# Kernel tuning notes

Hardware: AMD Instinct MI355X
Metric: run time of the kernel (lower is better)

## Reference

```python
import jax, jax.numpy as jnp
import numpy as np

B, S, D_IN = 4, 2048, 1024
N_HEAD, D_ATTN, D_OUT = 16, 64, 1024
D_H = N_HEAD * D_ATTN  # 1024; NOTE: no head split in original module


def setup_inputs() -> dict:
    key = jax.random.key(0)
    ks = jax.random.split(key, 12)
    s = 1.0 / np.sqrt(D_IN)
    inp = {
        "q": jax.random.normal(ks[0], (B, S, D_IN), dtype=jnp.float32),
        "k": jax.random.normal(ks[1], (B, S, D_IN), dtype=jnp.float32),
        "v": jax.random.normal(ks[2], (B, S, D_IN), dtype=jnp.float32),
        "mask": jax.random.randint(ks[3], (B, S, S), 0, 2, dtype=jnp.int32),
        "Wq": jax.random.normal(ks[4], (D_H, D_IN), dtype=jnp.float32) * s,
        "bq": jnp.zeros((D_H,), dtype=jnp.float32),
        "Wk": jax.random.normal(ks[5], (D_H, D_IN), dtype=jnp.float32) * s,
        "bk": jnp.zeros((D_H,), dtype=jnp.float32),
        "Wv": jax.random.normal(ks[6], (D_H, D_IN), dtype=jnp.float32) * s,
        "bv": jnp.zeros((D_H,), dtype=jnp.float32),
        "Wo": jax.random.normal(ks[7], (D_OUT, D_H), dtype=jnp.float32) * (1.0 / np.sqrt(D_H)),
        "bo": jnp.zeros((D_OUT,), dtype=jnp.float32),
    }
    return inp


def reference(q, k, v, mask, Wq, bq, Wk, bk, Wv, bv, Wo, bo):
    # manual QKV projections (torch Linear: x @ W.T + b)
    Q = q @ Wq.T + bq  # [B,S,D_H]
    K = k @ Wk.T + bk
    V = v @ Wv.T + bv
    d_k = Q.shape[-1]  # full concatenated dim (no head split, faithful)
    e = jnp.einsum("bsd,btd->bst", Q, K) / jnp.sqrt(jnp.float32(d_k))  # [B,S,S]
    MASK_FILL = jnp.float32(-(2 ** 15))  # original uses -2**15 regardless of dtype
    e = jnp.where(mask == 0, MASK_FILL, e)
    a = jax.nn.softmax(e, axis=-1)
    y = jnp.einsum("bst,btd->bsd", a, V)  # [B,S,D_H]
    return y @ Wo.T + bo  # [B,S,D_OUT]
```

## Files before the change

kernel.cpp:

```cpp
#include <hip/hip_runtime.h>
#include <hip/hip_bf16.h>

#define B_   4
#define S_   2048
#define DIN  1024
#define DH   1024
#define DOUT 1024

typedef __attribute__((ext_vector_type(8))) __bf16 bf16x8;
typedef __attribute__((ext_vector_type(4))) float floatx4;
typedef __attribute__((ext_vector_type(4))) float f32x4;
typedef __attribute__((ext_vector_type(4))) u_short u16x4;
typedef unsigned short u16;
typedef unsigned int u32;
typedef unsigned long long u64;

__device__ inline u16 f2bf(float f) {
  union { float f; u32 u; } x; x.f = f;
  u32 r = x.u + 0x7fffu + ((x.u >> 16) & 1u);
  return (u16)(r >> 16);
}

#define GLOAD(SRC, DST) __builtin_amdgcn_global_load_lds(                     \
    (const __attribute__((address_space(1))) u32*)(SRC),                      \
    (__attribute__((address_space(3))) u32*)(DST), 16, 0, 0)
#define WAITVM0() asm volatile("s_waitcnt vmcnt(0)" ::: "memory")

__global__ __launch_bounds__(256)
void cast_all(const float* __restrict__ q, const float* __restrict__ k,
              const float* __restrict__ v, const float* __restrict__ w0,
              const float* __restrict__ w1, const float* __restrict__ w2,
              const float* __restrict__ w3, u16* __restrict__ dst) {
  const long nQ = (long)B_ * S_ * DIN;
  const long nW = (long)DH * DIN;
  long b = blockIdx.x;
  const float* src; long doff;
  if (b < 8192)       { src = q;  doff = 0;            }
  else if (b < 16384) { src = k;  doff = nQ;     b -= 8192;  }
  else if (b < 24576) { src = v;  doff = 2 * nQ; b -= 16384; }
  else if (b < 25600) { src = w0; doff = 3 * nQ; b -= 24576; }
  else if (b < 26624) { src = w1; doff = 3 * nQ + nW;     b -= 25600; }
  else if (b < 27648) { src = w2; doff = 3 * nQ + 2 * nW; b -= 26624; }
  else                { src = w3; doff = 3 * nQ + 3 * nW; b -= 27648; }
  long i = b * 256 + threadIdx.x;
  f32x4 vv = __builtin_nontemporal_load(((const f32x4*)src) + i);
  u16x4 o;
  o.x = f2bf(vv.x); o.y = f2bf(vv.y); o.z = f2bf(vv.z); o.w = f2bf(vv.w);
  ((u16x4*)(dst + doff))[i] = o;
}

__global__ __launch_bounds__(256)
void mask_pack(const int* __restrict__ mask, u64* __restrict__ packed) {
  const long i = (long)blockIdx.x * 256 + threadIdx.x;
  const int mk = __builtin_nontemporal_load(mask + i);
  const u64 bal = __ballot(mk != 0);
  if ((threadIdx.x & 63) == 0) packed[i >> 6] = bal;
}

__global__ __launch_bounds__(256)
void transpose_bf16(const u16* __restrict__ in, u16* __restrict__ out) {
  __shared__ u16 t[32][33];
  const int b = blockIdx.z;
  const int r0 = blockIdx.y * 32, c0 = blockIdx.x * 32;
  const int tx = threadIdx.x & 31, ty = threadIdx.x >> 5;
  const u16* ib = in + (long)b * S_ * DH;
  u16* ob = out + (long)b * DH * S_;
#pragma unroll
  for (int i = 0; i < 4; ++i) {
    int r = ty + i * 8;
    t[r][tx] = ib[(long)(r0 + r) * DH + (c0 + tx)];
  }
  __syncthreads();
#pragma unroll
  for (int i = 0; i < 4; ++i) {
    int r = ty + i * 8;
    ob[(long)(c0 + r) * S_ + (r0 + tx)] = t[tx][r];
  }
}

#define EPI_BF16_BIAS     0
#define EPI_BF16_ROWSCALE 1
#define EPI_F32_BIAS      2

template <int EPI>
__global__ __launch_bounds__(256, 4)
void gemm97(const u16* __restrict__ A, const u16* __restrict__ Bm,
            void* __restrict__ C,
            const float* __restrict__ bias0, const float* __restrict__ bias1,
            const float* __restrict__ bias2,
            const float* __restrict__ Psum,
            int M, int N, int K,
            long sA, long sB, long sC,
            int nbx, int nby) {
  __shared__ u16 lds_[16384];
  __shared__ float invs_s[(EPI == EPI_BF16_ROWSCALE) ? 128 : 1];

  const int tid = threadIdx.x;
  const int w = tid >> 6, l = tid & 63;
  const int wr = w >> 1, wc = w & 1;
  const int lr = l & 15, q = l >> 4;

  const int flat = blockIdx.x;
  const int swz = (flat & 7) * ((int)gridDim.x >> 3) + (flat >> 3);
  const int bx = swz % nbx;
  const int rest = swz / nbx;
  const int by = rest % nby;
  const int bz = rest / nby;

  const long arow0 = (long)by * 128;
  const long bcol0 = (long)bx * 128;
  const u16* Ab = A + bz * sA + arow0 * K;
  const u16* Bb = Bm + bz * sB + bcol0 * K;
  const int nt = K >> 6;

  if constexpr (EPI == EPI_BF16_ROWSCALE) {
    if (tid < 128) {
      const float4* p = (const float4*)(Psum + ((long)bz * S_ + arow0 + tid) * 16);
      float4 a = p[0], b = p[1], c = p[2], d = p[3];
      float s = (a.x + a.y + a.z + a.w) + (b.x + b.y + b.z + b.w)
              + (c.x + c.y + c.z + c.w) + (d.x + d.y + d.z + d.w);
      invs_s[tid] = 1.0f / s;
    }
  }

  const int st_r = tid >> 3;
  const int st_ks = (tid & 7) ^ (st_r & 7);

  floatx4 acc[4][4] = {};

  for (int t = 0; t < nt; ++t) {
    const long k0 = (long)t << 6;
#pragma unroll
    for (int i = 0; i < 4; ++i)
      GLOAD(Ab + (long)(i * 32 + st_r) * K + k0 + st_ks * 8,
            &lds_[i * 2048 + tid * 8]);
#pragma unroll
    for (int i = 0; i < 4; ++i)
      GLOAD(Bb + (long)(i * 32 + st_r) * K + k0 + st_ks * 8,
            &lds_[8192 + i * 2048 + tid * 8]);
    WAITVM0();
    __syncthreads();

    bf16x8 a[4][2], b[4][2];
#pragma unroll
    for (int m = 0; m < 4; ++m)
#pragma unroll
      for (int kk = 0; kk < 2; ++kk) {
        const int r = wr * 64 + m * 16 + lr, s = kk * 4 + q;
        a[m][kk] = *(const bf16x8*)&lds_[r * 64 + ((s ^ (r & 7)) * 8)];
      }
#pragma unroll
    for (int n = 0; n < 4; ++n)
#pragma unroll
      for (int kk = 0; kk < 2; ++kk) {
        const int c = wc * 64 + n * 16 + lr, s = kk * 4 + q;
        b[n][kk] = *(const bf16x8*)&lds_[8192 + c * 64 + ((s ^ (c & 7)) * 8)];
      }
#pragma unroll
    for (int kk = 0; kk < 2; ++kk)
#pragma unroll
      for (int n = 0; n < 4; ++n)
#pragma unroll
        for (int m = 0; m < 4; ++m)
          acc[m][n] = __builtin_amdgcn_mfma_f32_16x16x32_bf16(
              a[m][kk], b[n][kk], acc[m][n], 0, 0, 0);
    __syncthreads();
  }

  const int r4 = q * 4;
  const float* bp = bias0;
  if constexpr (EPI == EPI_BF16_BIAS)
    bp = (bz == 0) ? bias0 : ((bz == 1) ? bias1 : bias2);
#pragma unroll
  for (int mf = 0; mf < 4; ++mf)
#pragma unroll
    for (int nf = 0; nf < 4; ++nf)
#pragma unroll
      for (int r = 0; r < 4; ++r) {
        const long row = arow0 + wr * 64 + mf * 16 + r4 + r;
        const long col = bcol0 + wc * 64 + nf * 16 + lr;
        float v = acc[mf][nf][r];
        if constexpr (EPI == EPI_BF16_BIAS) {
          v += bp[col];
          ((u16*)C)[bz * sC + row * N + col] = f2bf(v);
        } else if constexpr (EPI == EPI_BF16_ROWSCALE) {
          v *= invs_s[wr * 64 + mf * 16 + r4 + r];
          ((u16*)C)[bz * sC + row * N + col] = f2bf(v);
        } else {
          v += bp[col];
          ((float*)C)[bz * sC + row * N + col] = v;
        }
      }
}

__global__ __launch_bounds__(256, 4)
void pexp128(const u16* __restrict__ Q, const u16* __restrict__ Kb_,
             u16* __restrict__ P, const u32* __restrict__ packed,
             float* __restrict__ Psum) {
  __shared__ u16 lds_[16384];

  const int tid = threadIdx.x;
  const int w = tid >> 6, l = tid & 63;
  const int wr = w >> 1, wc = w & 1;
  const int lr = l & 15, q = l >> 4;

  const int flat = blockIdx.x;
  const int swz = (flat & 7) * ((int)gridDim.x >> 3) + (flat >> 3);
  const int bx = swz & 15;
  const int rest = swz >> 4;
  const int by = rest & 15;
  const int bz = rest >> 4;

  const long arow0 = (long)by * 128;
  const long bcol0 = (long)bx * 128;
  const int K = DH;
  const u16* Ab = Q + (long)bz * S_ * DH + arow0 * K;
  const u16* Bb = Kb_ + (long)bz * S_ * DH + bcol0 * K;

  const int st_r = tid >> 3;
  const int st_ks = (tid & 7) ^ (st_r & 7);

  floatx4 acc[4][4] = {};

#pragma unroll 4
  for (int t = 0; t < 16; ++t) {
    const long k0 = (long)t << 6;
#pragma unroll
    for (int i = 0; i < 4; ++i)
      GLOAD(Ab + (long)(i * 32 + st_r) * K + k0 + st_ks * 8,
            &lds_[i * 2048 + tid * 8]);
#pragma unroll
    for (int i = 0; i < 4; ++i)
      GLOAD(Bb + (long)(i * 32 + st_r) * K + k0 + st_ks * 8,
            &lds_[8192 + i * 2048 + tid * 8]);
    WAITVM0();
    __syncthreads();

    bf16x8 a[4][2], b[4][2];
#pragma unroll
    for (int m = 0; m < 4; ++m)
#pragma unroll
      for (int kk = 0; kk < 2; ++kk) {
        const int r = wr * 64 + m * 16 + lr, s = kk * 4 + q;
        a[m][kk] = *(const bf16x8*)&lds_[r * 64 + ((s ^ (r & 7)) * 8)];
      }
#pragma unroll
    for (int n = 0; n < 4; ++n)
#pragma unroll
      for (int kk = 0; kk < 2; ++kk) {
        const int c = wc * 64 + n * 16 + lr, s = kk * 4 + q;
        b[n][kk] = *(const bf16x8*)&lds_[8192 + c * 64 + ((s ^ (c & 7)) * 8)];
      }
#pragma unroll
    for (int kk = 0; kk < 2; ++kk)
#pragma unroll
      for (int n = 0; n < 4; ++n)
#pragma unroll
        for (int m = 0; m < 4; ++m)
          acc[m][n] = __builtin_amdgcn_mfma_f32_16x16x32_bf16(
              a[m][kk], b[n][kk], acc[m][n], 0, 0, 0);
    __syncthreads();
  }

  u32* pw = (u32*)&lds_[8192];
  {
    const u32* pg = packed + (long)bz * S_ * (S_ / 32)
                  + arow0 * (S_ / 32) + (bcol0 >> 5);
    const int lrow = tid >> 1;
    const int j0 = (tid & 1) * 2;
    pw[lrow * 4 + j0]     = pg[(long)lrow * (S_ / 32) + j0];
    pw[lrow * 4 + j0 + 1] = pg[(long)lrow * (S_ / 32) + j0 + 1];
  }
  __syncthreads();

  const int r4 = q * 4;
  float rsum[4][4];
#pragma unroll
  for (int mf = 0; mf < 4; ++mf)
#pragma unroll
    for (int r = 0; r < 4; ++r) rsum[mf][r] = 0.f;

#pragma unroll
  for (int mf = 0; mf < 4; ++mf)
#pragma unroll
    for (int r = 0; r < 4; ++r) {
      const int lrow = wr * 64 + mf * 16 + r4 + r;
      const long row = arow0 + lrow;
#pragma unroll
      for (int nf = 0; nf < 4; ++nf) {
        const u32 word = pw[lrow * 4 + wc * 2 + (nf >> 1)];
        const int bitpos = (nf & 1) * 16 + lr;
        const long col = bcol0 + wc * 64 + nf * 16 + lr;
        float p = 0.f;
        if ((word >> bitpos) & 1u) p = __expf(acc[mf][nf][r] * 0.03125f);
        P[(long)bz * S_ * S_ + row * S_ + col] = f2bf(p);
        rsum[mf][r] += p;
      }
    }
  __syncthreads();

  float* sc = (float*)lds_;
#pragma unroll
  for (int mf = 0; mf < 4; ++mf)
#pragma unroll
    for (int r = 0; r < 4; ++r) {
      float s = rsum[mf][r];
      s += __shfl_xor(s, 1); s += __shfl_xor(s, 2);
      s += __shfl_xor(s, 4); s += __shfl_xor(s, 8);
      if (lr == 0) sc[(wr * 64 + mf * 16 + r4 + r) * 2 + wc] = s;
    }
  __syncthreads();
  if (tid < 128) {
    float tot = sc[tid * 2] + sc[tid * 2 + 1];
    Psum[((long)bz * S_ + arow0 + tid) * 16 + bx] = tot;
  }
}

extern "C" void kernel_launch(void* const* d_in, const int* in_sizes, int n_in,
                              void* d_out, int out_size, void* d_ws, size_t ws_size,
                              hipStream_t stream) {
  const float* q    = (const float*)d_in[0];
  const float* k    = (const float*)d_in[1];
  const float* v    = (const float*)d_in[2];
  const int*   mask = (const int*)d_in[3];
  const float* Wq   = (const float*)d_in[4];
  const float* bq   = (const float*)d_in[5];
  const float* Wk   = (const float*)d_in[6];
  const float* bk   = (const float*)d_in[7];
  const float* Wv   = (const float*)d_in[8];
  const float* bv   = (const float*)d_in[9];
  const float* Wo   = (const float*)d_in[10];
  const float* bo   = (const float*)d_in[11];

  const long BS = (long)B_ * S_;
  const long nQ = BS * DH;
  const long nW = (long)DH * DIN;
  const long nE = (long)B_ * S_ * S_;

  char* ws = (char*)d_ws;
  size_t off = 0;
  auto alloc = [&](size_t bytes) {
    void* p = ws + off; off += (bytes + 255) & ~(size_t)255; return p;
  };

  u16* qb   = (u16*)alloc(nQ * 2);
  u16* kb   = (u16*)alloc(nQ * 2);
  u16* vb   = (u16*)alloc(nQ * 2);
  u16* wqb  = (u16*)alloc(nW * 2);
  u16* wkb  = (u16*)alloc(nW * 2);
  u16* wvb  = (u16*)alloc(nW * 2);
  u16* wob  = (u16*)alloc(nW * 2);
  u16* Qb   = (u16*)alloc(nQ * 2);
  u16* Kbf  = (u16*)alloc(nQ * 2);
  u16* Vb   = (u16*)alloc(nQ * 2);
  u16* VT   = (u16*)alloc(nQ * 2);
  u16* P    = (u16*)alloc(nE * 2);
  u64* pk   = (u64*)alloc(nE / 8);
  float* Psum = (float*)alloc(BS * 16 * 4);
  u16* Yb  = vb;
  (void)kb; (void)wkb; (void)wvb;

  cast_all<<<dim3(28672), 256, 0, stream>>>(q, k, v, Wq, Wk, Wv, Wo, qb);
  mask_pack<<<dim3(65536), 256, 0, stream>>>(mask, pk);

  gemm97<EPI_BF16_BIAS><<<dim3(1536), 256, 0, stream>>>(qb, wqb, Qb,
      bq, bk, bv, nullptr, (int)BS, DH, DIN, nQ, nW, nQ, 8, 64);

  {
    dim3 g(DH / 32, S_ / 32, B_);
    transpose_bf16<<<g, 256, 0, stream>>>(Vb, VT);
  }

  pexp128<<<dim3(1024), 256, 0, stream>>>(Qb, Kbf, P, (const u32*)pk, Psum);

  gemm97<EPI_BF16_ROWSCALE><<<dim3(512), 256, 0, stream>>>(P, VT, Yb,
      nullptr, nullptr, nullptr, Psum, S_, DH, S_,
      (long)S_ * S_, (long)DH * S_, (long)S_ * DH, 8, 16);

  gemm97<EPI_F32_BIAS><<<dim3(512), 256, 0, stream>>>(Yb, wob, d_out,
      bo, nullptr, nullptr, nullptr, (int)BS, DOUT, DH, 0, 0, 0, 8, 64);
}
```

Measured before the change: 235.4 us.

## Fuse fp32-to-bf16 activation cast into QKV projection GEMM and vectorize mask packing

```diff
diff --git a/kernel.cpp b/kernel.cpp
--- a/kernel.cpp
+++ b/kernel.cpp
@@ -10,6 +10,7 @@
 typedef __attribute__((ext_vector_type(8))) __bf16 bf16x8;
 typedef __attribute__((ext_vector_type(4))) float floatx4;
 typedef __attribute__((ext_vector_type(4))) float f32x4;
+typedef __attribute__((ext_vector_type(4))) int i32x4;
 typedef __attribute__((ext_vector_type(4))) u_short u16x4;
 typedef unsigned short u16;
 typedef unsigned int u32;
@@ -27,34 +28,35 @@
 #define WAITVM0() asm volatile("s_waitcnt vmcnt(0)" ::: "memory")
 
 __global__ __launch_bounds__(256)
-void cast_all(const float* __restrict__ q, const float* __restrict__ k,
-              const float* __restrict__ v, const float* __restrict__ w0,
-              const float* __restrict__ w1, const float* __restrict__ w2,
-              const float* __restrict__ w3, u16* __restrict__ dst) {
-  const long nQ = (long)B_ * S_ * DIN;
+void wcast(const float* __restrict__ w0, const float* __restrict__ w1,
+           const float* __restrict__ w2, const float* __restrict__ w3,
+           u16* __restrict__ dst) {
   const long nW = (long)DH * DIN;
   long b = blockIdx.x;
-  const float* src; long doff;
-  if (b < 8192)       { src = q;  doff = 0;            }
-  else if (b < 16384) { src = k;  doff = nQ;     b -= 8192;  }
-  else if (b < 24576) { src = v;  doff = 2 * nQ; b -= 16384; }
-  else if (b < 25600) { src = w0; doff = 3 * nQ; b -= 24576; }
-  else if (b < 26624) { src = w1; doff = 3 * nQ + nW;     b -= 25600; }
-  else if (b < 27648) { src = w2; doff = 3 * nQ + 2 * nW; b -= 26624; }
-  else                { src = w3; doff = 3 * nQ + 3 * nW; b -= 27648; }
-  long i = b * 256 + threadIdx.x;
+  const int r = (int)(b >> 10);
+  const float* src = (r == 0) ? w0 : (r == 1) ? w1 : (r == 2) ? w2 : w3;
+  long i = (b & 1023) * 256 + threadIdx.x;
   f32x4 vv = __builtin_nontemporal_load(((const f32x4*)src) + i);
   u16x4 o;
   o.x = f2bf(vv.x); o.y = f2bf(vv.y); o.z = f2bf(vv.z); o.w = f2bf(vv.w);
-  ((u16x4*)(dst + doff))[i] = o;
+  ((u16x4*)(dst + (long)r * nW))[i] = o;
 }
 
 __global__ __launch_bounds__(256)
 void mask_pack(const int* __restrict__ mask, u64* __restrict__ packed) {
-  const long i = (long)blockIdx.x * 256 + threadIdx.x;
-  const int mk = __builtin_nontemporal_load(mask + i);
-  const u64 bal = __ballot(mk != 0);
-  if ((threadIdx.x & 63) == 0) packed[i >> 6] = bal;
+  const long f = (long)blockIdx.x * 256 + threadIdx.x;
+  i32x4 m4 = __builtin_nontemporal_load(((const i32x4*)mask) + f);
+  u64 b0 = __ballot(m4.x != 0);
+  u64 b1 = __ballot(m4.y != 0);
+  u64 b2 = __ballot(m4.z != 0);
+  u64 b3 = __ballot(m4.w != 0);
+  if ((threadIdx.x & 63) == 0) {
+    const long g = f >> 6;
+    ulonglong2 p01; p01.x = b0; p01.y = b1;
+    ulonglong2 p23; p23.x = b2; p23.y = b3;
+    ((ulonglong2*)(packed + g * 4))[0] = p01;
+    ((ulonglong2*)(packed + g * 4))[1] = p23;
+  }
 }
 
 __global__ __launch_bounds__(256)
@@ -82,10 +84,12 @@
 #define EPI_BF16_ROWSCALE 1
 #define EPI_F32_BIAS      2
 
-template <int EPI>
+template <int EPI, bool AF32>
 __global__ __launch_bounds__(256, 4)
-void gemm97(const u16* __restrict__ A, const u16* __restrict__ Bm,
-            void* __restrict__ C,
+void gemm97(const u16* __restrict__ A,
+            const float* __restrict__ Af0, const float* __restrict__ Af1,
+            const float* __restrict__ Af2,
+            const u16* __restrict__ Bm, void* __restrict__ C,
             const float* __restrict__ bias0, const float* __restrict__ bias1,
             const float* __restrict__ bias2,
             const float* __restrict__ Psum,
@@ -109,7 +113,14 @@
 
   const long arow0 = (long)by * 128;
   const long bcol0 = (long)bx * 128;
-  const u16* Ab = A + bz * sA + arow0 * K;
+  const u16* Ab = nullptr;
+  const float* Afp = nullptr;
+  if constexpr (AF32) {
+    const float* As = (bz == 0) ? Af0 : ((bz == 1) ? Af1 : Af2);
+    Afp = As + arow0 * K;
+  } else {
+    Ab = A + bz * sA + arow0 * K;
+  }
   const u16* Bb = Bm + bz * sB + bcol0 * K;
   const int nt = K >> 6;
 
@@ -130,15 +141,40 @@
 
   for (int t = 0; t < nt; ++t) {
     const long k0 = (long)t << 6;
-#pragma unroll
-    for (int i = 0; i < 4; ++i)
-      GLOAD(Ab + (long)(i * 32 + st_r) * K + k0 + st_ks * 8,
-            &lds_[i * 2048 + tid * 8]);
-#pragma unroll
-    for (int i = 0; i < 4; ++i)
-      GLOAD(Bb + (long)(i * 32 + st_r) * K + k0 + st_ks * 8,
-            &lds_[8192 + i * 2048 + tid * 8]);
-    WAITVM0();
+    if constexpr (AF32) {
+      f32x4 va[4][2];
+#pragma unroll
+      for (int i = 0; i < 4; ++i) {
+        const float* sp = Afp + (long)(i * 32 + st_r) * K + k0 + st_ks * 8;
+        va[i][0] = *(const f32x4*)sp;
+        va[i][1] = *(const f32x4*)(sp + 4);
+      }
+#pragma unroll
+      for (int i = 0; i < 4; ++i)
+        GLOAD(Bb + (long)(i * 32 + st_r) * K + k0 + st_ks * 8,
+              &lds_[8192 + i * 2048 + tid * 8]);
+#pragma unroll
+      for (int i = 0; i < 4; ++i) {
+        bf16x8 o;
+#pragma unroll
+        for (int j = 0; j < 4; ++j) {
+          o[j]     = (__bf16)va[i][0][j];
+          o[j + 4] = (__bf16)va[i][1][j];
+        }
+        *(bf16x8*)&lds_[i * 2048 + tid * 8] = o;
+      }
+      WAITVM0();
+    } else {
+#pragma unroll
+      for (int i = 0; i < 4; ++i)
+        GLOAD(Ab + (long)(i * 32 + st_r) * K + k0 + st_ks * 8,
+              &lds_[i * 2048 + tid * 8]);
+#pragma unroll
+      for (int i = 0; i < 4; ++i)
+        GLOAD(Bb + (long)(i * 32 + st_r) * K + k0 + st_ks * 8,
+              &lds_[8192 + i * 2048 + tid * 8]);
+      WAITVM0();
+    }
     __syncthreads();
 
     bf16x8 a[4][2], b[4][2];
@@ -264,12 +300,12 @@
 
   u32* pw = (u32*)&lds_[8192];
   {
-    const u32* pg = packed + (long)bz * S_ * (S_ / 32)
-                  + arow0 * (S_ / 32) + (bcol0 >> 5);
+    const int half = bx & 1;
     const int lrow = tid >> 1;
     const int j0 = (tid & 1) * 2;
-    pw[lrow * 4 + j0]     = pg[(long)lrow * (S_ / 32) + j0];
-    pw[lrow * 4 + j0 + 1] = pg[(long)lrow * (S_ / 32) + j0 + 1];
+    const long g = (long)bz * 16384 + (arow0 + lrow) * 8 + (bx >> 1);
+    pw[lrow * 4 + j0]     = packed[g * 8 + j0 * 2 + half];
+    pw[lrow * 4 + j0 + 1] = packed[g * 8 + (j0 + 1) * 2 + half];
   }
   __syncthreads();
 
@@ -286,10 +322,10 @@
     for (int r = 0; r < 4; ++r) {
       const int lrow = wr * 64 + mf * 16 + r4 + r;
       const long row = arow0 + lrow;
+      const u32 word = pw[lrow * 4 + (lr & 3)];
 #pragma unroll
       for (int nf = 0; nf < 4; ++nf) {
-        const u32 word = pw[lrow * 4 + wc * 2 + (nf >> 1)];
-        const int bitpos = (nf & 1) * 16 + lr;
+        const int bitpos = wc * 16 + nf * 4 + (lr >> 2);
         const long col = bcol0 + wc * 64 + nf * 16 + lr;
         float p = 0.f;
         if ((word >> bitpos) & 1u) p = __expf(acc[mf][nf][r] * 0.03125f);
@@ -343,13 +379,7 @@
     void* p = ws + off; off += (bytes + 255) & ~(size_t)255; return p;
   };
 
-  u16* qb   = (u16*)alloc(nQ * 2);
-  u16* kb   = (u16*)alloc(nQ * 2);
-  u16* vb   = (u16*)alloc(nQ * 2);
-  u16* wqb  = (u16*)alloc(nW * 2);
-  u16* wkb  = (u16*)alloc(nW * 2);
-  u16* wvb  = (u16*)alloc(nW * 2);
-  u16* wob  = (u16*)alloc(nW * 2);
+  u16* wqb  = (u16*)alloc(4 * nW * 2);
   u16* Qb   = (u16*)alloc(nQ * 2);
   u16* Kbf  = (u16*)alloc(nQ * 2);
   u16* Vb   = (u16*)alloc(nQ * 2);
@@ -357,14 +387,16 @@
   u16* P    = (u16*)alloc(nE * 2);
   u64* pk   = (u64*)alloc(nE / 8);
   float* Psum = (float*)alloc(BS * 16 * 4);
-  u16* Yb  = vb;
-  (void)kb; (void)wkb; (void)wvb;
-
-  cast_all<<<dim3(28672), 256, 0, stream>>>(q, k, v, Wq, Wk, Wv, Wo, qb);
-  mask_pack<<<dim3(65536), 256, 0, stream>>>(mask, pk);
-
-  gemm97<EPI_BF16_BIAS><<<dim3(1536), 256, 0, stream>>>(qb, wqb, Qb,
-      bq, bk, bv, nullptr, (int)BS, DH, DIN, nQ, nW, nQ, 8, 64);
+  u16* Yb   = (u16*)alloc(nQ * 2);
+  u16* wob  = wqb + 3 * nW;
+  (void)Kbf;
+
+  wcast<<<dim3(4096), 256, 0, stream>>>(Wq, Wk, Wv, Wo, wqb);
+  mask_pack<<<dim3(16384), 256, 0, stream>>>(mask, pk);
+
+  gemm97<EPI_BF16_BIAS, true><<<dim3(1536), 256, 0, stream>>>(
+      nullptr, q, k, v, wqb, Qb, bq, bk, bv, nullptr,
+      (int)BS, DH, DIN, 0, nW, nQ, 8, 64);
 
   {
     dim3 g(DH / 32, S_ / 32, B_);
@@ -373,10 +405,11 @@
 
   pexp128<<<dim3(1024), 256, 0, stream>>>(Qb, Kbf, P, (const u32*)pk, Psum);
 
-  gemm97<EPI_BF16_ROWSCALE><<<dim3(512), 256, 0, stream>>>(P, VT, Yb,
-      nullptr, nullptr, nullptr, Psum, S_, DH, S_,
-      (long)S_ * S_, (long)DH * S_, (long)S_ * DH, 8, 16);
-
-  gemm97<EPI_F32_BIAS><<<dim3(512), 256, 0, stream>>>(Yb, wob, d_out,
-      bo, nullptr, nullptr, nullptr, (int)BS, DOUT, DH, 0, 0, 0, 8, 64);
-}
+  gemm97<EPI_BF16_ROWSCALE, false><<<dim3(512), 256, 0, stream>>>(
+      P, nullptr, nullptr, nullptr, VT, Yb, nullptr, nullptr, nullptr, Psum,
+      S_, DH, S_, (long)S_ * S_, (long)DH * S_, (long)S_ * DH, 8, 16);
+
+  gemm97<EPI_F32_BIAS, false><<<dim3(512), 256, 0, stream>>>(
+      Yb, nullptr, nullptr, nullptr, wob, d_out, bo, nullptr, nullptr, nullptr,
+      (int)BS, DOUT, DH, 0, 0, 0, 8, 64);
+}
```

After: 241.2 us. 1.02x slower.

## Fuse fp32-to-bf16 activation cast into QKV projection GEMM A-tile loads

Applied to the files above, without the earlier changes.

```diff
diff --git a/kernel.cpp b/kernel.cpp
--- a/kernel.cpp
+++ b/kernel.cpp
@@ -27,26 +27,18 @@
 #define WAITVM0() asm volatile("s_waitcnt vmcnt(0)" ::: "memory")
 
 __global__ __launch_bounds__(256)
-void cast_all(const float* __restrict__ q, const float* __restrict__ k,
-              const float* __restrict__ v, const float* __restrict__ w0,
-              const float* __restrict__ w1, const float* __restrict__ w2,
-              const float* __restrict__ w3, u16* __restrict__ dst) {
-  const long nQ = (long)B_ * S_ * DIN;
+void wcast(const float* __restrict__ w0, const float* __restrict__ w1,
+           const float* __restrict__ w2, const float* __restrict__ w3,
+           u16* __restrict__ dst) {
   const long nW = (long)DH * DIN;
   long b = blockIdx.x;
-  const float* src; long doff;
-  if (b < 8192)       { src = q;  doff = 0;            }
-  else if (b < 16384) { src = k;  doff = nQ;     b -= 8192;  }
-  else if (b < 24576) { src = v;  doff = 2 * nQ; b -= 16384; }
-  else if (b < 25600) { src = w0; doff = 3 * nQ; b -= 24576; }
-  else if (b < 26624) { src = w1; doff = 3 * nQ + nW;     b -= 25600; }
-  else if (b < 27648) { src = w2; doff = 3 * nQ + 2 * nW; b -= 26624; }
-  else                { src = w3; doff = 3 * nQ + 3 * nW; b -= 27648; }
-  long i = b * 256 + threadIdx.x;
+  const int r = (int)(b >> 10);
+  const float* src = (r == 0) ? w0 : (r == 1) ? w1 : (r == 2) ? w2 : w3;
+  long i = (b & 1023) * 256 + threadIdx.x;
   f32x4 vv = __builtin_nontemporal_load(((const f32x4*)src) + i);
   u16x4 o;
   o.x = f2bf(vv.x); o.y = f2bf(vv.y); o.z = f2bf(vv.z); o.w = f2bf(vv.w);
-  ((u16x4*)(dst + doff))[i] = o;
+  ((u16x4*)(dst + (long)r * nW))[i] = o;
 }
 
 __global__ __launch_bounds__(256)
@@ -78,7 +70,110 @@
   }
 }
 
-#define EPI_BF16_BIAS     0
+__global__ __launch_bounds__(256, 3)
+void gemm97f(const float* __restrict__ Af0, const float* __restrict__ Af1,
+             const float* __restrict__ Af2,
+             const u16* __restrict__ Bm, u16* __restrict__ C,
+             const float* __restrict__ bias0, const float* __restrict__ bias1,
+             const float* __restrict__ bias2,
+             int M, int N, int K, long sB, long sC,
+             int nbx, int nby) {
+  __shared__ u16 lds_[24576];
+
+  const int tid = threadIdx.x;
+  const int w = tid >> 6, l = tid & 63;
+  const int wr = w >> 1, wc = w & 1;
+  const int lr = l & 15, q = l >> 4;
+
+  const int flat = blockIdx.x;
+  const int swz = (flat & 7) * ((int)gridDim.x >> 3) + (flat >> 3);
+  const int bx = swz % nbx;
+  const int rest = swz / nbx;
+  const int by = rest % nby;
+  const int bz = rest / nby;
+
+  const long arow0 = (long)by * 128;
+  const long bcol0 = (long)bx * 128;
+  const float* As = (bz == 0) ? Af0 : ((bz == 1) ? Af1 : Af2);
+  const float* Afp = As + arow0 * K;
+  const u16* Bb = Bm + bz * sB + bcol0 * K;
+  const int nt = K >> 6;
+
+  const int stA_r = tid >> 4;
+  const int stA_c = tid & 15;
+  const int stB_r = tid >> 3;
+  const int stB_ks = (tid & 7) ^ (stB_r & 7);
+
+  floatx4 acc[4][4] = {};
+
+  for (int t = 0; t < nt; ++t) {
+    const long k0 = (long)t << 6;
+#pragma unroll
+    for (int i = 0; i < 8; ++i) {
+      const int row = i * 16 + stA_r;
+      const int csw = stA_c ^ (row & 15);
+      GLOAD(Afp + (long)row * K + k0 + csw * 4,
+            &lds_[i * 2048 + tid * 8]);
+    }
+#pragma unroll
+    for (int i = 0; i < 4; ++i)
+      GLOAD(Bb + (long)(i * 32 + stB_r) * K + k0 + stB_ks * 8,
+            &lds_[16384 + i * 2048 + tid * 8]);
+    WAITVM0();
+    __syncthreads();
+
+    bf16x8 a[4][2], b[4][2];
+#pragma unroll
+    for (int m = 0; m < 4; ++m)
+#pragma unroll
+      for (int kk = 0; kk < 2; ++kk) {
+        const int r = wr * 64 + m * 16 + lr;
+        const int s8 = kk * 4 + q;
+        const int c0 = (2 * s8) ^ (r & 15);
+        const int c1 = (2 * s8 + 1) ^ (r & 15);
+        f32x4 lo = *(const f32x4*)&lds_[r * 128 + c0 * 8];
+        f32x4 hi = *(const f32x4*)&lds_[r * 128 + c1 * 8];
+        bf16x8 o;
+#pragma unroll
+        for (int j = 0; j < 4; ++j) {
+          o[j]     = (__bf16)lo[j];
+          o[j + 4] = (__bf16)hi[j];
+        }
+        a[m][kk] = o;
+      }
+#pragma unroll
+    for (int n = 0; n < 4; ++n)
+#pragma unroll
+      for (int kk = 0; kk < 2; ++kk) {
+        const int c = wc * 64 + n * 16 + lr, s = kk * 4 + q;
+        b[n][kk] = *(const bf16x8*)&lds_[16384 + c * 64 + ((s ^ (c & 7)) * 8)];
+      }
+#pragma unroll
+    for (int kk = 0; kk < 2; ++kk)
+#pragma unroll
+      for (int n = 0; n < 4; ++n)
+#pragma unroll
+        for (int m = 0; m < 4; ++m)
+          acc[m][n] = __builtin_amdgcn_mfma_f32_16x16x32_bf16(
+              a[m][kk], b[n][kk], acc[m][n], 0, 0, 0);
+    __syncthreads();
+  }
+
+  const int r4 = q * 4;
+  const float* bp = (bz == 0) ? bias0 : ((bz == 1) ? bias1 : bias2);
+#pragma unroll
+  for (int mf = 0; mf < 4; ++mf)
+#pragma unroll
+    for (int nf = 0; nf < 4; ++nf)
+#pragma unroll
+      for (int r = 0; r < 4; ++r) {
+        const long row = arow0 + wr * 64 + mf * 16 + r4 + r;
+        const long col = bcol0 + wc * 64 + nf * 16 + lr;
+        float v = acc[mf][nf][r] + bp[col];
+        C[bz * sC + row * N + col] = f2bf(v);
+      }
+}
+
 #define EPI_BF16_ROWSCALE 1
 #define EPI_F32_BIAS      2
 
@@ -86,8 +181,7 @@
 __global__ __launch_bounds__(256, 4)
 void gemm97(const u16* __restrict__ A, const u16* __restrict__ Bm,
             void* __restrict__ C,
-            const float* __restrict__ bias0, const float* __restrict__ bias1,
-            const float* __restrict__ bias2,
+            const float* __restrict__ bias0,
             const float* __restrict__ Psum,
             int M, int N, int K,
             long sA, long sB, long sC,
@@ -168,9 +262,6 @@
   }
 
   const int r4 = q * 4;
-  const float* bp = bias0;
-  if constexpr (EPI == EPI_BF16_BIAS)
-    bp = (bz == 0) ? bias0 : ((bz == 1) ? bias1 : bias2);
 #pragma unroll
   for (int mf = 0; mf < 4; ++mf)
 #pragma unroll
@@ -180,14 +271,11 @@
         const long row = arow0 + wr * 64 + mf * 16 + r4 + r;
         const long col = bcol0 + wc * 64 + nf * 16 + lr;
         float v = acc[mf][nf][r];
-        if constexpr (EPI == EPI_BF16_BIAS) {
-          v += bp[col];
-          ((u16*)C)[bz * sC + row * N + col] = f2bf(v);
-        } else if constexpr (EPI == EPI_BF16_ROWSCALE) {
+        if constexpr (EPI == EPI_BF16_ROWSCALE) {
           v *= invs_s[wr * 64 + mf * 16 + r4 + r];
           ((u16*)C)[bz * sC + row * N + col] = f2bf(v);
         } else {
-          v += bp[col];
+          v += bias0[col];
           ((float*)C)[bz * sC + row * N + col] = v;
         }
       }
@@ -343,13 +431,7 @@
     void* p = ws + off; off += (bytes + 255) & ~(size_t)255; return p;
   };
 
-  u16* qb   = (u16*)alloc(nQ * 2);
-  u16* kb   = (u16*)alloc(nQ * 2);
-  u16* vb   = (u16*)alloc(nQ * 2);
-  u16* wqb  = (u16*)alloc(nW * 2);
-  u16* wkb  = (u16*)alloc(nW * 2);
-  u16* wvb  = (u16*)alloc(nW * 2);
-  u16* wob  = (u16*)alloc(nW * 2);
+  u16* wqb  = (u16*)alloc(4 * nW * 2);
   u16* Qb   = (u16*)alloc(nQ * 2);
   u16* Kbf  = (u16*)alloc(nQ * 2);
   u16* Vb   = (u16*)alloc(nQ * 2);
@@ -357,14 +439,14 @@
   u16* P    = (u16*)alloc(nE * 2);
   u64* pk   = (u64*)alloc(nE / 8);
   float* Psum = (float*)alloc(BS * 16 * 4);
-  u16* Yb  = vb;
-  (void)kb; (void)wkb; (void)wvb;
-
-  cast_all<<<dim3(28672), 256, 0, stream>>>(q, k, v, Wq, Wk, Wv, Wo, qb);
+  u16* Yb   = (u16*)alloc(nQ * 2);
+  u16* wob  = wqb + 3 * nW;
+
+  wcast<<<dim3(4096), 256, 0, stream>>>(Wq, Wk, Wv, Wo, wqb);
   mask_pack<<<dim3(65536), 256, 0, stream>>>(mask, pk);
 
-  gemm97<EPI_BF16_BIAS><<<dim3(1536), 256, 0, stream>>>(qb, wqb, Qb,
-      bq, bk, bv, nullptr, (int)BS, DH, DIN, nQ, nW, nQ, 8, 64);
+  gemm97f<<<dim3(1536), 256, 0, stream>>>(q, k, v, wqb, Qb, bq, bk, bv,
+      (int)BS, DH, DIN, nW, nQ, 8, 64);
 
   {
     dim3 g(DH / 32, S_ / 32, B_);
@@ -374,9 +456,9 @@
   pexp128<<<dim3(1024), 256, 0, stream>>>(Qb, Kbf, P, (const u32*)pk, Psum);
 
   gemm97<EPI_BF16_ROWSCALE><<<dim3(512), 256, 0, stream>>>(P, VT, Yb,
-      nullptr, nullptr, nullptr, Psum, S_, DH, S_,
+      nullptr, Psum, S_, DH, S_,
       (long)S_ * S_, (long)DH * S_, (long)S_ * DH, 8, 16);
 
   gemm97<EPI_F32_BIAS><<<dim3(512), 256, 0, stream>>>(Yb, wob, d_out,
-      bo, nullptr, nullptr, nullptr, (int)BS, DOUT, DH, 0, 0, 0, 8, 64);
-}
+      bo, nullptr, (int)BS, DOUT, DH, 0, 0, 0, 8, 64);
+}
```

New measurement: 227.9 us. 3.2% less time.
